# Kernel optimization log

Measured on AMD Instinct MI355X. Metric: run time of the kernel, lower is better.

Reference implementation:

```python
import jax, jax.numpy as jnp
import numpy as np

NUM_BUCKETS = 32
MAX_DISTANCE = 128
N_HEADS = 16
D_KV = 64


def relative_position_bucket(rel, num_buckets=NUM_BUCKETS, max_distance=MAX_DISTANCE):
    # bidirectional (encoder) bucketing, matches the torch reference
    nb = num_buckets // 2
    ret = (rel > 0).astype(jnp.int32) * nb
    rp = jnp.abs(rel)
    max_exact = nb // 2
    is_small = rp < max_exact
    # guard log(0); masked out by is_small anyway
    large = max_exact + (
        jnp.log(jnp.maximum(rp, 1).astype(jnp.float32) / max_exact)
        / np.log(max_distance / max_exact)
        * (nb - max_exact)
    ).astype(jnp.int32)
    large = jnp.minimum(large, nb - 1)
    return ret + jnp.where(is_small, rp, large)


def compute_bias(rel_bias_table, q_len, k_len):
    q_pos = jnp.arange(q_len)[:, None]
    k_pos = jnp.arange(k_len)[None, :]
    buckets = relative_position_bucket(k_pos - q_pos)  # [S, K]
    bias = rel_bias_table[buckets]                      # [S, K, H]
    return jnp.transpose(bias, (2, 0, 1))[None]         # [1, H, S, K]


def setup_inputs() -> dict:
    key = jax.random.key(0)
    ks = jax.random.split(key, 6)
    d_model, inner = 1024, N_HEADS * D_KV
    scale = 1.0 / np.sqrt(d_model)
    return {
        "hidden_states": jax.random.normal(ks[0], (4, 2048, d_model), jnp.float32),
        "Wq": jax.random.normal(ks[1], (d_model, inner), jnp.float32) * scale,
        "Wk": jax.random.normal(ks[2], (d_model, inner), jnp.float32) * scale,
        "Wv": jax.random.normal(ks[3], (d_model, inner), jnp.float32) * scale,
        "Wo": jax.random.normal(ks[4], (inner, d_model), jnp.float32) * scale,
        "rel_bias_table": jax.random.normal(ks[5], (NUM_BUCKETS, N_HEADS), jnp.float32),
    }


def reference(hidden_states, Wq, Wk, Wv, Wo, rel_bias_table):
    B, S, _ = hidden_states.shape
    K_len = S  # self-attention (key_value_states is None)
    q = (hidden_states @ Wq).reshape(B, S, N_HEADS, D_KV)
    k = (hidden_states @ Wk).reshape(B, K_len, N_HEADS, D_KV)
    v = (hidden_states @ Wv).reshape(B, K_len, N_HEADS, D_KV)
    # NOTE: T5 attention has no 1/sqrt(d_kv) scaling
    scores = jnp.einsum("bshd,bkhd->bhsk", q, k)
    pos_bias = compute_bias(rel_bias_table, S, K_len)
    attn = jax.nn.softmax(scores + pos_bias, axis=-1)
    out = jnp.einsum("bhsk,bkhd->bshd", attn, v).reshape(B, S, N_HEADS * D_KV)
    out = out @ Wo
    return (out, pos_bias)
```

## Files before the change

kernel.cpp:

```cpp
#include <hip/hip_runtime.h>
#include <cstdint>
#include <cstddef>

typedef unsigned short u16;
typedef unsigned int u32;
typedef __attribute__((ext_vector_type(8))) short bf16x8;
typedef __attribute__((ext_vector_type(4))) float f32x4;
typedef __attribute__((ext_vector_type(16))) float f32x16;
typedef __attribute__((ext_vector_type(2))) unsigned int u32x2;

#define MFMA(a, b, c)   __builtin_amdgcn_mfma_f32_16x16x32_bf16((a), (b), (c), 0, 0, 0)
#define MFMA32(a, b, c) __builtin_amdgcn_mfma_f32_32x32x16_bf16((a), (b), (c), 0, 0, 0)

typedef const __attribute__((address_space(1))) void gv1_t;
typedef __attribute__((address_space(3))) void lv3_t;
#define GLOAD_LDS16(g, l) __builtin_amdgcn_global_load_lds((gv1_t*)(g), (lv3_t*)(l), 16, 0, 0)

#define BATCH 4
#define SEQ 2048
#define DMODEL 1024
#define NHEAD 16
#define MROWS (BATCH * SEQ)
#define QKVN (3 * DMODEL)

#define LOG2E 1.44269504088896340736f

__device__ __forceinline__ u16 f2bf(float f) {
  u32 x = __builtin_bit_cast(u32, f);
  x += 0x7fffu + ((x >> 16) & 1u);
  return (u16)(x >> 16);
}

__device__ __forceinline__ u32 pkbf(float a, float b) {
  return (u32)f2bf(a) | ((u32)f2bf(b) << 16);
}

__device__ __forceinline__ u32 pkbf_fast(float a, float b) {
  u32 au = __builtin_bit_cast(u32, a) + 0x8000u;
  u32 bu = __builtin_bit_cast(u32, b) + 0x8000u;
  return __builtin_amdgcn_perm(bu, au, 0x07060302u);
}

__device__ __forceinline__ u32x2 plswap(u32 a, u32 b) {
  return __builtin_amdgcn_permlane32_swap(a, b, false, false);
}

extern "C" __device__ float __ocml_exp2_f32(float);
__device__ __forceinline__ float exp2fast(float x) {
#if __has_builtin(__builtin_amdgcn_exp2f)
  return __builtin_amdgcn_exp2f(x);
#else
  return __ocml_exp2_f32(x);
#endif
}

__global__ __launch_bounds__(256) void convert_h(const float* __restrict__ H,
                                                 u16* __restrict__ Hb) {
  size_t i = (size_t)blockIdx.x * 1024 + threadIdx.x * 4;
  float4 v = *(const float4*)&H[i];
  uint2 o;
  o.x = pkbf(v.x, v.y);
  o.y = pkbf(v.z, v.w);
  *(uint2*)&Hb[i] = o;
}

__global__ void transpose_w(const float* __restrict__ Wq, const float* __restrict__ Wk,
                            const float* __restrict__ Wv, const float* __restrict__ Wo,
                            u16* __restrict__ Wt) {
  __shared__ u16 Ts[32][33];
  const float* W = (blockIdx.z == 0) ? Wq : (blockIdx.z == 1) ? Wk
                   : (blockIdx.z == 2) ? Wv : Wo;
  const float s = (blockIdx.z == 0) ? LOG2E : 1.0f;
  int x = threadIdx.x, y0 = threadIdx.y;
  int r0 = blockIdx.y * 32, c0 = blockIdx.x * 32;
  for (int yy = y0; yy < 32; yy += 8)
    Ts[yy][x] = f2bf(W[(size_t)(r0 + yy) * 1024 + c0 + x] * s);
  __syncthreads();
  for (int yy = y0; yy < 32; yy += 8)
    Wt[(size_t)(blockIdx.z * 1024 + c0 + yy) * 1024 + r0 + x] = Ts[x][yy];
}

__device__ __forceinline__ int rel_bucket(int rel) {
  int ret = (rel > 0) ? 16 : 0;
  int rp = (rel < 0) ? -rel : rel;
  if (rp < 8) return ret + rp;
  int i = 0;
  i += (rp >= 12); i += (rp >= 16); i += (rp >= 23); i += (rp >= 32);
  i += (rp >= 46); i += (rp >= 64); i += (rp >= 91);
  return ret + 8 + i;
}

__global__ __launch_bounds__(256) void build_bias_rel(const float* __restrict__ tbl,
                                                      float* __restrict__ brel,
                                                      float* __restrict__ brel2) {
  int h = blockIdx.x;
  for (int rix = threadIdx.x; rix < 4095; rix += 256) {
    float v = tbl[rel_bucket(rix - 2047) * NHEAD + h];
    brel[h * 4096 + rix] = v;
    brel2[h * 4096 + rix] = v * LOG2E;
  }
}

__global__ __launch_bounds__(256) void gemm_bf16k(const u16* __restrict__ A,
                                                  const u16* __restrict__ Bt,
                                                  u16* __restrict__ Cb, float* __restrict__ Cf,
                                                  u16* __restrict__ Vt,
                                                  int M, int N, int K) {
  __shared__ u16 As[128 * 32];
  __shared__ u16 Bs[128 * 32];
  const int t = threadIdx.x;
  const int w = t >> 6, lane = t & 63, quad = lane >> 4, l15 = lane & 15;
  const int wr = w >> 1, wc = w & 1;

  const int nwg = gridDim.x * gridDim.y;
  const int orig = blockIdx.y * gridDim.x + blockIdx.x;
  const int wg = (orig & 7) * (nwg >> 3) + (orig >> 3);
  const int bx = wg % gridDim.x, by = wg / gridDim.x;
  const int row0 = by * 128, col0 = bx * 128;

  f32x4 acc[4][4];
  #pragma unroll
  for (int i = 0; i < 4; ++i)
    #pragma unroll
    for (int j = 0; j < 4; ++j) acc[i][j] = (f32x4){0.f, 0.f, 0.f, 0.f};

  const int srow = lane >> 2, scol = (lane & 3) * 8;

  for (int k0 = 0; k0 < K; k0 += 32) {
    #pragma unroll
    for (int p = 0; p < 2; ++p) {
      const int rb = w * 32 + p * 16;
      GLOAD_LDS16(&A[(size_t)(row0 + rb + srow) * K + k0 + scol], &As[rb * 32]);
      GLOAD_LDS16(&Bt[(size_t)(col0 + rb + srow) * K + k0 + scol], &Bs[rb * 32]);
    }
    __syncthreads();
    bf16x8 af[4], bfr[4];
    #pragma unroll
    for (int i = 0; i < 4; ++i)
      af[i] = *(const bf16x8*)&As[(wr * 64 + i * 16 + l15) * 32 + quad * 8];
    #pragma unroll
    for (int j = 0; j < 4; ++j)
      bfr[j] = *(const bf16x8*)&Bs[(wc * 64 + j * 16 + l15) * 32 + quad * 8];
    #pragma unroll
    for (int i = 0; i < 4; ++i)
      #pragma unroll
      for (int j = 0; j < 4; ++j)
        acc[i][j] = MFMA(af[i], bfr[j], acc[i][j]);
    __syncthreads();
  }
  #pragma unroll
  for (int i = 0; i < 4; ++i) {
    #pragma unroll
    for (int j = 0; j < 4; ++j) {
      const int col = col0 + wc * 64 + j * 16 + l15;
      const int srow0 = row0 + wr * 64 + i * 16 + quad * 4;
      if (Cf) {
        #pragma unroll
        for (int r = 0; r < 4; ++r)
          Cf[(size_t)(srow0 + r) * N + col] = acc[i][j][r];
      } else if (!Vt || col < 2 * DMODEL) {
        #pragma unroll
        for (int r = 0; r < 4; ++r)
          Cb[(size_t)(srow0 + r) * N + col] = f2bf(acc[i][j][r]);
      } else {
        const int c2 = col - 2 * DMODEL, hh = c2 >> 6, dd = c2 & 63;
        const int bb = srow0 >> 11, ss = srow0 & (SEQ - 1);
        uint2 o;
        o.x = pkbf(acc[i][j][0], acc[i][j][1]);
        o.y = pkbf(acc[i][j][2], acc[i][j][3]);
        *(uint2*)&Vt[((size_t)(bb * 16 + hh) * 64 + dd) * SEQ + ss] = o;
      }
    }
  }
}

__global__ __launch_bounds__(256) void attn_fused(const u16* __restrict__ QKV,
                                                  const u16* __restrict__ Vt,
                                                  const float* __restrict__ brel,
                                                  const float* __restrict__ brel2,
                                                  u16* __restrict__ Aout,
                                                  float* __restrict__ pb) {
  __shared__ u16 Ks[2][64 * 72];
  __shared__ u16 Vs[2][64 * 72];
  const int orig = blockIdx.y * gridDim.x + blockIdx.x;
  const int wg = (orig & 7) * 128 + (orig >> 3);
  const int qt = wg & 15, bh = wg >> 4;
  const int b = bh >> 4, h = bh & 15;
  const int t = threadIdx.x;
  const int w = t >> 6, lane = t & 63, l31 = lane & 31, h5 = lane >> 5;
  const int qb = qt * 128;
  const int qw0 = qb + w * 32;
  const int qr = qw0 + l31;

  const float cpos = brel2[h * 4096 + 4040];
  const float cneg = brel2[h * 4096 + 54];
  const float cpu  = brel[h * 4096 + 4040];
  const float cnu  = brel[h * 4096 + 54];

  const u16* qptr = QKV + (size_t)(b * SEQ + qr) * QKVN + h * 64 + h5 * 8;
  bf16x8 qf[4];
  #pragma unroll
  for (int ks = 0; ks < 4; ++ks) qf[ks] = *(const bf16x8*)(qptr + ks * 16);

  float lsum = 0.f;
  f32x16 oacc[2];
  #pragma unroll
  for (int m = 0; m < 2; ++m)
    #pragma unroll
    for (int i = 0; i < 16; ++i) oacc[m][i] = 0.f;

  const int c0 = t * 2, c1 = c0 + 1;
  const int r0s = c0 >> 3, cc0 = (c0 & 7) * 8;
  const int r1s = c1 >> 3, cc1 = (c1 & 7) * 8;
  const size_t krow = (size_t)(b * SEQ) * QKVN + DMODEL + h * 64;
  const size_t vtrow = (size_t)bh * 64;
  const float* brow = brel2 + h * 4096 + 2047;

  uint4 ka0 = *(const uint4*)&QKV[krow + (size_t)r0s * QKVN + cc0];
  uint4 ka1 = *(const uint4*)&QKV[krow + (size_t)r1s * QKVN + cc1];
  uint4 va0 = *(const uint4*)&Vt[(vtrow + r0s) * SEQ + cc0];
  uint4 va1 = *(const uint4*)&Vt[(vtrow + r1s) * SEQ + cc1];
  *(uint4*)&Ks[0][r0s * 72 + cc0] = ka0;
  *(uint4*)&Ks[0][r1s * 72 + cc1] = ka1;
  *(uint4*)&Vs[0][r0s * 72 + cc0] = va0;
  *(uint4*)&Vs[0][r1s * 72 + cc1] = va1;
  __syncthreads();

  #pragma unroll 2
  for (int ti = 0; ti < SEQ / 64; ++ti) {
    const int kb = ti * 64;
    const int cur = ti & 1;
    const u16* Kc = Ks[cur];
    const u16* Vc = Vs[cur];

    if (ti + 1 < SEQ / 64) {
      ka0 = *(const uint4*)&QKV[krow + (size_t)(kb + 64 + r0s) * QKVN + cc0];
      ka1 = *(const uint4*)&QKV[krow + (size_t)(kb + 64 + r1s) * QKVN + cc1];
      va0 = *(const uint4*)&Vt[(vtrow + r0s) * SEQ + kb + 64 + cc0];
      va1 = *(const uint4*)&Vt[(vtrow + r1s) * SEQ + kb + 64 + cc1];
    }

    bf16x8 bp[4];
    #pragma unroll
    for (int m = 0; m < 2; ++m) {
      f32x16 sc;
      #pragma unroll
      for (int i = 0; i < 16; ++i) sc[i] = 0.f;
      __builtin_amdgcn_s_setprio(1);
      #pragma unroll
      for (int ks = 0; ks < 4; ++ks) {
        bf16x8 kf = *(const bf16x8*)&Kc[(m * 32 + l31) * 72 + ks * 16 + h5 * 8];
        sc = MFMA32(kf, qf[ks], sc);
      }
      __builtin_amdgcn_s_setprio(0);

      if (m == 0 && (ti & 3) == b) {
        const int pr = qb + (t >> 1);
        const int pc = kb + (t & 1) * 32;
        float* po = pb + ((size_t)(h * SEQ + pr)) * SEQ + pc;
        const int lo = pc - pr;
        if (lo >= 91 || lo + 31 <= -91) {
          const float c = (lo >= 91) ? cpu : cnu;
          const float4 vv = {c, c, c, c};
          #pragma unroll
          for (int i = 0; i < 8; ++i) *(float4*)&po[i * 4] = vv;
        } else {
          const float* bb = brel + h * 4096 + 2047 - pr + pc;
          #pragma unroll
          for (int i = 0; i < 8; ++i) {
            float4 vv;
            vv.x = bb[i * 4]; vv.y = bb[i * 4 + 1];
            vv.z = bb[i * 4 + 2]; vv.w = bb[i * 4 + 3];
            *(float4*)&po[i * 4] = vv;
          }
        }
      }

      const int kb32 = kb + 32 * m;
      if (kb32 >= qw0 + 122) {
        #pragma unroll
        for (int i = 0; i < 16; ++i) sc[i] += cpos;
      } else if (kb32 <= qw0 - 122) {
        #pragma unroll
        for (int i = 0; i < 16; ++i) sc[i] += cneg;
      } else {
        const float* bb = brow + kb32 + 4 * h5 - qr;
        #pragma unroll
        for (int i = 0; i < 16; ++i) sc[i] += bb[(i & 3) + 8 * (i >> 2)];
      }
      u32 w0[4], w1[4];
      #pragma unroll
      for (int tt = 0; tt < 4; ++tt) {
        float p0 = exp2fast(sc[4 * tt + 0]);
        float p1 = exp2fast(sc[4 * tt + 1]);
        float p2 = exp2fast(sc[4 * tt + 2]);
        float p3 = exp2fast(sc[4 * tt + 3]);
        lsum += (p0 + p1) + (p2 + p3);
        w0[tt] = pkbf_fast(p0, p1);
        w1[tt] = pkbf_fast(p2, p3);
      }
      u32x2 r0 = plswap(w0[0], w0[1]);
      u32x2 r1 = plswap(w1[0], w1[1]);
      u32x2 r2 = plswap(w0[2], w0[3]);
      u32x2 r3 = plswap(w1[2], w1[3]);
      union { u32 u[4]; bf16x8 v; } q0, q1;
      q0.u[0] = r0.x; q0.u[1] = r1.x; q0.u[2] = r0.y; q0.u[3] = r1.y;
      q1.u[0] = r2.x; q1.u[1] = r3.x; q1.u[2] = r2.y; q1.u[3] = r3.y;
      bp[2 * m]     = q0.v;
      bp[2 * m + 1] = q1.v;
    }

    __builtin_amdgcn_s_setprio(1);
    #pragma unroll
    for (int m2 = 0; m2 < 2; ++m2)
      #pragma unroll
      for (int ks = 0; ks < 4; ++ks) {
        bf16x8 vf = *(const bf16x8*)&Vc[(m2 * 32 + l31) * 72 + ks * 16 + h5 * 8];
        oacc[m2] = MFMA32(vf, bp[ks], oacc[m2]);
      }
    __builtin_amdgcn_s_setprio(0);

    if (ti + 1 < SEQ / 64) {
      u16* Kn = Ks[cur ^ 1];
      u16* Vn = Vs[cur ^ 1];
      *(uint4*)&Kn[r0s * 72 + cc0] = ka0;
      *(uint4*)&Kn[r1s * 72 + cc1] = ka1;
      *(uint4*)&Vn[r0s * 72 + cc0] = va0;
      *(uint4*)&Vn[r1s * 72 + cc1] = va1;
    }
    __syncthreads();
  }

  lsum += __shfl_xor(lsum, 32);
  const float inv = 1.0f / lsum;
  const size_t rowb = (size_t)(b * SEQ + qr) * DMODEL + h * 64;
  #pragma unroll
  for (int m2 = 0; m2 < 2; ++m2)
    #pragma unroll
    for (int tt = 0; tt < 4; ++tt) {
      uint2 o;
      o.x = pkbf(oacc[m2][4 * tt + 0] * inv, oacc[m2][4 * tt + 1] * inv);
      o.y = pkbf(oacc[m2][4 * tt + 2] * inv, oacc[m2][4 * tt + 3] * inv);
      *(uint2*)&Aout[rowb + 32 * m2 + 8 * tt + 4 * h5] = o;
    }
}

extern "C" void kernel_launch(void* const* d_in, const int* in_sizes, int n_in,
                              void* d_out, int out_size, void* d_ws, size_t ws_size,
                              hipStream_t stream) {
  (void)in_sizes; (void)n_in; (void)out_size; (void)ws_size;
  const float* H   = (const float*)d_in[0];
  const float* Wq  = (const float*)d_in[1];
  const float* Wk  = (const float*)d_in[2];
  const float* Wv  = (const float*)d_in[3];
  const float* Wo  = (const float*)d_in[4];
  const float* tbl = (const float*)d_in[5];

  float* out = (float*)d_out;
  float* pos_bias = out + (size_t)MROWS * DMODEL;

  char* ws = (char*)d_ws;
  u16* Hb     = (u16*)(ws);
  u16* Wt     = (u16*)(ws + 16777216);
  u16* QKV    = (u16*)(ws + 25165824);
  u16* Vt     = (u16*)(ws + 75497472);
  float* brel  = (float*)(ws + 92274688);
  float* brel2 = (float*)(ws + 92536832);

  convert_h<<<8192, 256, 0, stream>>>(H, Hb);
  transpose_w<<<dim3(32, 32, 4), dim3(32, 8), 0, stream>>>(Wq, Wk, Wv, Wo, Wt);
  build_bias_rel<<<16, 256, 0, stream>>>(tbl, brel, brel2);

  gemm_bf16k<<<dim3(QKVN / 128, MROWS / 128), 256, 0, stream>>>(
      Hb, Wt, QKV, nullptr, Vt, MROWS, QKVN, DMODEL);
  attn_fused<<<dim3(16, 64), 256, 0, stream>>>(QKV, Vt, brel, brel2,
                                               Hb , pos_bias);
  gemm_bf16k<<<dim3(DMODEL / 128, MROWS / 128), 256, 0, stream>>>(
      Hb, Wt + (size_t)QKVN * DMODEL, nullptr, out, nullptr, MROWS, DMODEL, DMODEL);
}
```

Measured before the change: 558.7 us.

## Stage K/V tiles via direct global-to-LDS loads with XOR swizzle

Replaces the register round-trip staging of K and V tiles (global load into registers, then LDS store after compute) with global_load_lds direct DMA into the next double buffer. The padded 72-stride layout becomes an unpadded 64-stride layout, with an XOR swizzle on the source column and on the read address to avoid bank conflicts. This frees VGPRs and removes the LDS write instructions. It relies on the single end-of-iteration barrier being enough to order the async LDS writes, and on the swizzle mapping matching the per-lane destination layout.

```diff
diff --git a/kernel.cpp b/kernel.cpp
--- a/kernel.cpp
+++ b/kernel.cpp
@@ -180,8 +180,8 @@
                                                   const float* __restrict__ brel2,
                                                   u16* __restrict__ Aout,
                                                   float* __restrict__ pb) {
-  __shared__ u16 Ks[2][64 * 72];
-  __shared__ u16 Vs[2][64 * 72];
+  __shared__ u16 Ks[2][64 * 64];
+  __shared__ u16 Vs[2][64 * 64];
   const int orig = blockIdx.y * gridDim.x + blockIdx.x;
   const int wg = (orig & 7) * 128 + (orig >> 3);
   const int qt = wg & 15, bh = wg >> 4;
@@ -209,21 +209,26 @@
     #pragma unroll
     for (int i = 0; i < 16; ++i) oacc[m][i] = 0.f;
 
-  const int c0 = t * 2, c1 = c0 + 1;
-  const int r0s = c0 >> 3, cc0 = (c0 & 7) * 8;
-  const int r1s = c1 >> 3, cc1 = (c1 & 7) * 8;
   const size_t krow = (size_t)(b * SEQ) * QKVN + DMODEL + h * 64;
   const size_t vtrow = (size_t)bh * 64;
   const float* brow = brel2 + h * 4096 + 2047;
 
-  uint4 ka0 = *(const uint4*)&QKV[krow + (size_t)r0s * QKVN + cc0];
-  uint4 ka1 = *(const uint4*)&QKV[krow + (size_t)r1s * QKVN + cc1];
-  uint4 va0 = *(const uint4*)&Vt[(vtrow + r0s) * SEQ + cc0];
-  uint4 va1 = *(const uint4*)&Vt[(vtrow + r1s) * SEQ + cc1];
-  *(uint4*)&Ks[0][r0s * 72 + cc0] = ka0;
-  *(uint4*)&Ks[0][r1s * 72 + cc1] = ka1;
-  *(uint4*)&Vs[0][r0s * 72 + cc0] = va0;
-  *(uint4*)&Vs[0][r1s * 72 + cc1] = va1;
+  const int srccol = ((lane & 7) * 8) ^ ((lane >> 3) << 3);
+  const int swz = (l31 & 7) << 3;
+
+  #define STAGE_TILE(buf, kb64)                                                  \
+    {                                                                            \
+      _Pragma("unroll")                                                          \
+      for (int p = 0; p < 2; ++p) {                                              \
+        const int rr = (w * 2 + p) * 8 + (lane >> 3);                            \
+        GLOAD_LDS16(&QKV[krow + (size_t)((kb64) + rr) * QKVN + srccol],          \
+                    &Ks[buf][(w * 2 + p) * 512]);                                \
+        GLOAD_LDS16(&Vt[(vtrow + rr) * SEQ + (kb64) + srccol],                   \
+                    &Vs[buf][(w * 2 + p) * 512]);                                \
+      }                                                                          \
+    }
+
+  STAGE_TILE(0, 0);
   __syncthreads();
 
   #pragma unroll 2
@@ -233,12 +238,7 @@
     const u16* Kc = Ks[cur];
     const u16* Vc = Vs[cur];
 
-    if (ti + 1 < SEQ / 64) {
-      ka0 = *(const uint4*)&QKV[krow + (size_t)(kb + 64 + r0s) * QKVN + cc0];
-      ka1 = *(const uint4*)&QKV[krow + (size_t)(kb + 64 + r1s) * QKVN + cc1];
-      va0 = *(const uint4*)&Vt[(vtrow + r0s) * SEQ + kb + 64 + cc0];
-      va1 = *(const uint4*)&Vt[(vtrow + r1s) * SEQ + kb + 64 + cc1];
-    }
+    if (ti + 1 < SEQ / 64) STAGE_TILE(cur ^ 1, kb + 64);
 
     bf16x8 bp[4];
     #pragma unroll
@@ -249,7 +249,7 @@
       __builtin_amdgcn_s_setprio(1);
       #pragma unroll
       for (int ks = 0; ks < 4; ++ks) {
-        bf16x8 kf = *(const bf16x8*)&Kc[(m * 32 + l31) * 72 + ks * 16 + h5 * 8];
+        bf16x8 kf = *(const bf16x8*)&Kc[(m * 32 + l31) * 64 + ((ks * 16 + h5 * 8) ^ swz)];
         sc = MFMA32(kf, qf[ks], sc);
       }
       __builtin_amdgcn_s_setprio(0);
@@ -315,19 +315,11 @@
     for (int m2 = 0; m2 < 2; ++m2)
       #pragma unroll
       for (int ks = 0; ks < 4; ++ks) {
-        bf16x8 vf = *(const bf16x8*)&Vc[(m2 * 32 + l31) * 72 + ks * 16 + h5 * 8];
+        bf16x8 vf = *(const bf16x8*)&Vc[(m2 * 32 + l31) * 64 + ((ks * 16 + h5 * 8) ^ swz)];
         oacc[m2] = MFMA32(vf, bp[ks], oacc[m2]);
       }
     __builtin_amdgcn_s_setprio(0);
 
-    if (ti + 1 < SEQ / 64) {
-      u16* Kn = Ks[cur ^ 1];
-      u16* Vn = Vs[cur ^ 1];
-      *(uint4*)&Kn[r0s * 72 + cc0] = ka0;
-      *(uint4*)&Kn[r1s * 72 + cc1] = ka1;
-      *(uint4*)&Vn[r0s * 72 + cc0] = va0;
-      *(uint4*)&Vn[r1s * 72 + cc1] = va1;
-    }
     __syncthreads();
   }
 
```

Measured after the change: 567.7 us. Within noise of the previous version (+1.6%).

## Split attention KV range in two halves with separate combine kernel

Applied to the files above, without the earlier changes.

Adds a split-KV attention variant in which each workgroup processes half of the key/value sequence. This doubles the grid to 2048 blocks. Unnormalized fp32 partial outputs and row sums are written to workspace, and a new combine kernel sums the two halves, normalizes and writes the bf16 attention output. The aim is more parallelism and better load balancing across CUs. The cost is an extra kernel launch plus roughly 64MB of fp32 partials written and read back. The split path only runs if the workspace is large enough; otherwise the original kernel is used.

```diff
diff --git a/kernel.cpp b/kernel.cpp
--- a/kernel.cpp
+++ b/kernel.cpp
@@ -174,12 +174,13 @@
   }
 }
 
-__global__ __launch_bounds__(256) void attn_fused(const u16* __restrict__ QKV,
-                                                  const u16* __restrict__ Vt,
-                                                  const float* __restrict__ brel,
-                                                  const float* __restrict__ brel2,
-                                                  u16* __restrict__ Aout,
-                                                  float* __restrict__ pb) {
+
+__global__ __launch_bounds__(256) void attn_full(const u16* __restrict__ QKV,
+                                                 const u16* __restrict__ Vt,
+                                                 const float* __restrict__ brel,
+                                                 const float* __restrict__ brel2,
+                                                 u16* __restrict__ Aout,
+                                                 float* __restrict__ pb) {
   __shared__ u16 Ks[2][64 * 72];
   __shared__ u16 Vs[2][64 * 72];
   const int orig = blockIdx.y * gridDim.x + blockIdx.x;
@@ -345,10 +346,208 @@
     }
 }
 
+__global__ __launch_bounds__(256) void attn_split(const u16* __restrict__ QKV,
+                                                  const u16* __restrict__ Vt,
+                                                  const float* __restrict__ brel,
+                                                  const float* __restrict__ brel2,
+                                                  float* __restrict__ Opart,
+                                                  float* __restrict__ lpart,
+                                                  float* __restrict__ pb) {
+  __shared__ u16 Ks[2][64 * 72];
+  __shared__ u16 Vs[2][64 * 72];
+  const int orig = blockIdx.y * gridDim.x + blockIdx.x;
+  const int wg = (orig & 7) * 256 + (orig >> 3);
+  const int qt = wg & 15, bh2 = wg >> 4;
+  const int bh = bh2 >> 1, half = bh2 & 1;
+  const int b = bh >> 4, h = bh & 15;
+  const int kvbase = half << 10;
+  const int t = threadIdx.x;
+  const int w = t >> 6, lane = t & 63, l31 = lane & 31, h5 = lane >> 5;
+  const int qb = qt * 128;
+  const int qw0 = qb + w * 32;
+  const int qr = qw0 + l31;
+
+  const float cpos = brel2[h * 4096 + 4040];
+  const float cneg = brel2[h * 4096 + 54];
+  const float cpu  = brel[h * 4096 + 4040];
+  const float cnu  = brel[h * 4096 + 54];
+
+  const u16* qptr = QKV + (size_t)(b * SEQ + qr) * QKVN + h * 64 + h5 * 8;
+  bf16x8 qf[4];
+  #pragma unroll
+  for (int ks = 0; ks < 4; ++ks) qf[ks] = *(const bf16x8*)(qptr + ks * 16);
+
+  float lsum = 0.f;
+  f32x16 oacc[2];
+  #pragma unroll
+  for (int m = 0; m < 2; ++m)
+    #pragma unroll
+    for (int i = 0; i < 16; ++i) oacc[m][i] = 0.f;
+
+  const int c0 = t * 2, c1 = c0 + 1;
+  const int r0s = c0 >> 3, cc0 = (c0 & 7) * 8;
+  const int r1s = c1 >> 3, cc1 = (c1 & 7) * 8;
+  const size_t krow = (size_t)(b * SEQ) * QKVN + DMODEL + h * 64;
+  const size_t vtrow = (size_t)bh * 64;
+  const float* brow = brel2 + h * 4096 + 2047;
+
+  uint4 ka0 = *(const uint4*)&QKV[krow + (size_t)(kvbase + r0s) * QKVN + cc0];
+  uint4 ka1 = *(const uint4*)&QKV[krow + (size_t)(kvbase + r1s) * QKVN + cc1];
+  uint4 va0 = *(const uint4*)&Vt[(vtrow + r0s) * SEQ + kvbase + cc0];
+  uint4 va1 = *(const uint4*)&Vt[(vtrow + r1s) * SEQ + kvbase + cc1];
+  *(uint4*)&Ks[0][r0s * 72 + cc0] = ka0;
+  *(uint4*)&Ks[0][r1s * 72 + cc1] = ka1;
+  *(uint4*)&Vs[0][r0s * 72 + cc0] = va0;
+  *(uint4*)&Vs[0][r1s * 72 + cc1] = va1;
+  __syncthreads();
+
+  #pragma unroll 2
+  for (int ti = 0; ti < 16; ++ti) {
+    const int kb = kvbase + ti * 64;
+    const int cur = ti & 1;
+    const u16* Kc = Ks[cur];
+    const u16* Vc = Vs[cur];
+
+    if (ti + 1 < 16) {
+      ka0 = *(const uint4*)&QKV[krow + (size_t)(kb + 64 + r0s) * QKVN + cc0];
+      ka1 = *(const uint4*)&QKV[krow + (size_t)(kb + 64 + r1s) * QKVN + cc1];
+      va0 = *(const uint4*)&Vt[(vtrow + r0s) * SEQ + kb + 64 + cc0];
+      va1 = *(const uint4*)&Vt[(vtrow + r1s) * SEQ + kb + 64 + cc1];
+    }
+
+    bf16x8 bp[4];
+    #pragma unroll
+    for (int m = 0; m < 2; ++m) {
+      f32x16 sc;
+      #pragma unroll
+      for (int i = 0; i < 16; ++i) sc[i] = 0.f;
+      __builtin_amdgcn_s_setprio(1);
+      #pragma unroll
+      for (int ks = 0; ks < 4; ++ks) {
+        bf16x8 kf = *(const bf16x8*)&Kc[(m * 32 + l31) * 72 + ks * 16 + h5 * 8];
+        sc = MFMA32(kf, qf[ks], sc);
+      }
+      __builtin_amdgcn_s_setprio(0);
+
+      if (m == 0 && (ti & 3) == b) {
+        const int pr = qb + (t >> 1);
+        const int pc = kb + (t & 1) * 32;
+        float* po = pb + ((size_t)(h * SEQ + pr)) * SEQ + pc;
+        const int lo = pc - pr;
+        if (lo >= 91 || lo + 31 <= -91) {
+          const float c = (lo >= 91) ? cpu : cnu;
+          const float4 vv = {c, c, c, c};
+          #pragma unroll
+          for (int i = 0; i < 8; ++i) *(float4*)&po[i * 4] = vv;
+        } else {
+          const float* bb = brel + h * 4096 + 2047 - pr + pc;
+          #pragma unroll
+          for (int i = 0; i < 8; ++i) {
+            float4 vv;
+            vv.x = bb[i * 4]; vv.y = bb[i * 4 + 1];
+            vv.z = bb[i * 4 + 2]; vv.w = bb[i * 4 + 3];
+            *(float4*)&po[i * 4] = vv;
+          }
+        }
+      }
+
+      const int kb32 = kb + 32 * m;
+      if (kb32 >= qw0 + 122) {
+        #pragma unroll
+        for (int i = 0; i < 16; ++i) sc[i] += cpos;
+      } else if (kb32 <= qw0 - 122) {
+        #pragma unroll
+        for (int i = 0; i < 16; ++i) sc[i] += cneg;
+      } else {
+        const float* bb = brow + kb32 + 4 * h5 - qr;
+        #pragma unroll
+        for (int i = 0; i < 16; ++i) sc[i] += bb[(i & 3) + 8 * (i >> 2)];
+      }
+      u32 w0[4], w1[4];
+      #pragma unroll
+      for (int tt = 0; tt < 4; ++tt) {
+        float p0 = exp2fast(sc[4 * tt + 0]);
+        float p1 = exp2fast(sc[4 * tt + 1]);
+        float p2 = exp2fast(sc[4 * tt + 2]);
+        float p3 = exp2fast(sc[4 * tt + 3]);
+        lsum += (p0 + p1) + (p2 + p3);
+        w0[tt] = pkbf_fast(p0, p1);
+        w1[tt] = pkbf_fast(p2, p3);
+      }
+      u32x2 r0 = plswap(w0[0], w0[1]);
+      u32x2 r1 = plswap(w1[0], w1[1]);
+      u32x2 r2 = plswap(w0[2], w0[3]);
+      u32x2 r3 = plswap(w1[2], w1[3]);
+      union { u32 u[4]; bf16x8 v; } q0, q1;
+      q0.u[0] = r0.x; q0.u[1] = r1.x; q0.u[2] = r0.y; q0.u[3] = r1.y;
+      q1.u[0] = r2.x; q1.u[1] = r3.x; q1.u[2] = r2.y; q1.u[3] = r3.y;
+      bp[2 * m]     = q0.v;
+      bp[2 * m + 1] = q1.v;
+    }
+
+    __builtin_amdgcn_s_setprio(1);
+    #pragma unroll
+    for (int m2 = 0; m2 < 2; ++m2)
+      #pragma unroll
+      for (int ks = 0; ks < 4; ++ks) {
+        bf16x8 vf = *(const bf16x8*)&Vc[(m2 * 32 + l31) * 72 + ks * 16 + h5 * 8];
+        oacc[m2] = MFMA32(vf, bp[ks], oacc[m2]);
+      }
+    __builtin_amdgcn_s_setprio(0);
+
+    if (ti + 1 < 16) {
+      u16* Kn = Ks[cur ^ 1];
+      u16* Vn = Vs[cur ^ 1];
+      *(uint4*)&Kn[r0s * 72 + cc0] = ka0;
+      *(uint4*)&Kn[r1s * 72 + cc1] = ka1;
+      *(uint4*)&Vn[r0s * 72 + cc0] = va0;
+      *(uint4*)&Vn[r1s * 72 + cc1] = va1;
+    }
+    __syncthreads();
+  }
+
+  lsum += __shfl_xor(lsum, 32);
+  if (h5 == 0) lpart[(size_t)bh2 * SEQ + qr] = lsum;
+  const size_t orow = ((size_t)bh2 * SEQ + qr) * 64;
+  #pragma unroll
+  for (int m2 = 0; m2 < 2; ++m2)
+    #pragma unroll
+    for (int tt = 0; tt < 4; ++tt) {
+      f32x4 v = {oacc[m2][4 * tt + 0], oacc[m2][4 * tt + 1],
+                 oacc[m2][4 * tt + 2], oacc[m2][4 * tt + 3]};
+      *(f32x4*)&Opart[orow + 32 * m2 + 8 * tt + 4 * h5] = v;
+    }
+}
+
+__global__ __launch_bounds__(256) void combine_o(const float* __restrict__ Opart,
+                                                 const float* __restrict__ lpart,
+                                                 u16* __restrict__ Aout) {
+  const int tid = blockIdx.x * 256 + threadIdx.x;
+  const int dg = tid & 7;
+  const int q  = (tid >> 3) & (SEQ - 1);
+  const int bh = tid >> 14;
+  const int b = bh >> 4, h = bh & 15;
+  const size_t o1 = ((size_t)(bh * 2 + 0) * SEQ + q) * 64 + dg * 8;
+  const size_t o2 = ((size_t)(bh * 2 + 1) * SEQ + q) * 64 + dg * 8;
+  const float l = lpart[(size_t)(bh * 2) * SEQ + q] +
+                  lpart[(size_t)(bh * 2 + 1) * SEQ + q];
+  const float inv = 1.0f / l;
+  float4 a0 = *(const float4*)&Opart[o1];
+  float4 a1 = *(const float4*)&Opart[o1 + 4];
+  float4 b0 = *(const float4*)&Opart[o2];
+  float4 b1 = *(const float4*)&Opart[o2 + 4];
+  uint4 o;
+  o.x = pkbf((a0.x + b0.x) * inv, (a0.y + b0.y) * inv);
+  o.y = pkbf((a0.z + b0.z) * inv, (a0.w + b0.w) * inv);
+  o.z = pkbf((a1.x + b1.x) * inv, (a1.y + b1.y) * inv);
+  o.w = pkbf((a1.z + b1.z) * inv, (a1.w + b1.w) * inv);
+  *(uint4*)&Aout[((size_t)(b * SEQ + q)) * DMODEL + h * 64 + dg * 8] = o;
+}
+
 extern "C" void kernel_launch(void* const* d_in, const int* in_sizes, int n_in,
                               void* d_out, int out_size, void* d_ws, size_t ws_size,
                               hipStream_t stream) {
-  (void)in_sizes; (void)n_in; (void)out_size; (void)ws_size;
+  (void)in_sizes; (void)n_in; (void)out_size;
   const float* H   = (const float*)d_in[0];
   const float* Wq  = (const float*)d_in[1];
   const float* Wk  = (const float*)d_in[2];
@@ -366,6 +565,9 @@
   u16* Vt     = (u16*)(ws + 75497472);
   float* brel  = (float*)(ws + 92274688);
   float* brel2 = (float*)(ws + 92536832);
+  float* Opart = (float*)(ws + 100663296);
+  float* lpart = (float*)(ws + 167772160);
+  const size_t ws_need_split = 167772160ull + 1048576ull;
 
   convert_h<<<8192, 256, 0, stream>>>(H, Hb);
   transpose_w<<<dim3(32, 32, 4), dim3(32, 8), 0, stream>>>(Wq, Wk, Wv, Wo, Wt);
@@ -373,8 +575,16 @@
 
   gemm_bf16k<<<dim3(QKVN / 128, MROWS / 128), 256, 0, stream>>>(
       Hb, Wt, QKV, nullptr, Vt, MROWS, QKVN, DMODEL);
-  attn_fused<<<dim3(16, 64), 256, 0, stream>>>(QKV, Vt, brel, brel2,
-                                               Hb , pos_bias);
+
+  if (ws_size >= ws_need_split) {
+    attn_split<<<dim3(16, 128), 256, 0, stream>>>(QKV, Vt, brel, brel2,
+                                                  Opart, lpart, pos_bias);
+    combine_o<<<4096, 256, 0, stream>>>(Opart, lpart, Hb );
+  } else {
+    attn_full<<<dim3(16, 64), 256, 0, stream>>>(QKV, Vt, brel, brel2,
+                                                Hb , pos_bias);
+  }
+
   gemm_bf16k<<<dim3(DMODEL / 128, MROWS / 128), 256, 0, stream>>>(
       Hb, Wt + (size_t)QKVN * DMODEL, nullptr, out, nullptr, MROWS, DMODEL, DMODEL);
 }
```

After: 575.4 us. 1.03x slower.
